# Performance work log

Measured on AMD Instinct MI355X. Metric: run time of the kernel, lower is better.

The kernel has to match this reference:

```python
import jax, jax.numpy as jnp
import numpy as np

N_NODES = 100000
N_EDGES = 2000000
N_GRAPHS = 2000
IN_DIM = 7
EDGE_DIM = 4
HID = 32
N_CLASSES = 2
NEG_SLOPE = 0.2
BN_EPS = 1e-5


def setup_inputs() -> dict:
    key = jax.random.key(0)
    ks = jax.random.split(key, 16)
    x = jax.random.normal(ks[0], (N_NODES, IN_DIM), dtype=jnp.float32)
    edge_index = jax.random.randint(ks[1], (2, N_EDGES), 0, N_NODES, dtype=jnp.int64)
    batch = jnp.sort(jax.random.randint(ks[2], (N_NODES,), 0, N_GRAPHS, dtype=jnp.int64))
    edge_attr = jax.random.normal(ks[3], (N_EDGES, EDGE_DIM), dtype=jnp.float32)
    s = 0.1
    W0 = jax.random.normal(ks[4], (IN_DIM, HID), dtype=jnp.float32) * s
    W12 = jax.random.normal(ks[5], (2, HID, HID), dtype=jnp.float32) * s
    att_src = jax.random.normal(ks[6], (3, HID), dtype=jnp.float32) * s
    att_dst = jax.random.normal(ks[7], (3, HID), dtype=jnp.float32) * s
    lin_edge = jax.random.normal(ks[8], (3, EDGE_DIM, HID), dtype=jnp.float32) * s
    att_edge = jax.random.normal(ks[9], (3, HID), dtype=jnp.float32) * s
    bias = jnp.zeros((3, HID), dtype=jnp.float32)
    bn_gamma = jnp.ones((3, HID), dtype=jnp.float32)
    bn_beta = jnp.zeros((3, HID), dtype=jnp.float32)
    fc_W = jax.random.normal(ks[10], (HID, N_CLASSES), dtype=jnp.float32) * s
    fc_b = jnp.zeros((N_CLASSES,), dtype=jnp.float32)
    return dict(x=x, edge_index=edge_index, batch=batch, edge_attr=edge_attr,
                W0=W0, W12=W12, att_src=att_src, att_dst=att_dst,
                lin_edge=lin_edge, att_edge=att_edge, bias=bias,
                bn_gamma=bn_gamma, bn_beta=bn_beta, fc_W=fc_W, fc_b=fc_b)


def gat_layer(x, src, dst, edge_attr, W, a_src, a_dst, We, a_edge, b):
    # PyG GATConv, heads=1, add_self_loops=False: edge_attr conditions attention only.
    N = x.shape[0]
    h = x @ W                                   # [N, H]
    e = edge_attr @ We                          # [E, H]
    score = ((h * a_src).sum(-1)[src]
             + (h * a_dst).sum(-1)[dst]
             + (e * a_edge).sum(-1))            # [E]
    score = jax.nn.leaky_relu(score, NEG_SLOPE)
    m = jax.ops.segment_max(score, dst, num_segments=N)
    w = jnp.exp(score - m[dst])
    denom = jax.ops.segment_sum(w, dst, num_segments=N)
    alpha = w / (denom[dst] + 1e-16)            # segment softmax over incoming edges
    out = jax.ops.segment_sum(h[src] * alpha[:, None], dst, num_segments=N)
    return out + b


def batchnorm(x, gamma, beta):
    mu = x.mean(axis=0)
    var = ((x - mu) ** 2).mean(axis=0)          # biased var, as torch BN normalization
    return (x - mu) * jax.lax.rsqrt(var + BN_EPS) * gamma + beta


def reference(x, edge_index, batch, edge_attr, W0, W12, att_src, att_dst,
              lin_edge, att_edge, bias, bn_gamma, bn_beta, fc_W, fc_b):
    src, dst = edge_index[0], edge_index[1]
    Ws = [W0, W12[0], W12[1]]
    h = x
    for l in range(3):
        h = gat_layer(h, src, dst, edge_attr, Ws[l], att_src[l], att_dst[l],
                      lin_edge[l], att_edge[l], bias[l])
        h = batchnorm(h, bn_gamma[l], bn_beta[l])
        h = jax.nn.relu(h)
    node_embs = h
    graph_emb = jax.ops.segment_sum(node_embs, batch, num_segments=N_GRAPHS)
    out = graph_emb @ fc_W + fc_b
    return (out, node_embs, graph_emb)
```

## Files before the change

### kernel.cpp

```cpp
#include <hip/hip_runtime.h>
#include <math.h>

#define N_NODES   100000
#define N_EDGES   2000000
#define N_GRAPHS  2000
#define IN_DIM    7
#define EDGE_DIM  4
#define HID       32
#define N_CLASSES 2
#define NEG_SLOPE 0.2f
#define BN_EPS    1e-5f

__global__ void k_ce_all(const float* __restrict__ lin_edge, const float* __restrict__ att_edge,
                         float* __restrict__ ce3, float* __restrict__ gsum3,
                         float* __restrict__ gsq3) {
    int t = threadIdx.x;
    if (t < 12) {
        int l = t >> 2, d = t & 3;
        float s = 0.f;
        for (int k = 0; k < HID; ++k)
            s += lin_edge[(size_t)l * EDGE_DIM * HID + d * HID + k] * att_edge[l * HID + k];
        ce3[t] = s;
    }
    if (t < 3 * HID) { gsum3[t] = 0.f; gsq3[t] = 0.f; }
}

__global__ void k_hist(const int* __restrict__ dst, int* __restrict__ deg) {
    int e = blockIdx.x * blockDim.x + threadIdx.x;
    if (e < N_EDGES) atomicAdd(deg + dst[e], 1);
}

__global__ void k_scan(const int* __restrict__ deg, int* __restrict__ offs,
                       int* __restrict__ cursor) {
    __shared__ int wsum[16];
    __shared__ int carry;
    int t = threadIdx.x, lane = t & 63, w = t >> 6;
    if (t == 0) carry = 0;
    __syncthreads();
    for (int base = 0; base < N_NODES; base += 1024) {
        int i = base + t;
        int v = (i < N_NODES) ? deg[i] : 0;
        int x = v;
#pragma unroll
        for (int o = 1; o < 64; o <<= 1) {
            int y = __shfl_up(x, o, 64);
            if (lane >= o) x += y;
        }
        if (lane == 63) wsum[w] = x;
        __syncthreads();
        if (t < 16) {
            int s = wsum[t];
#pragma unroll
            for (int o = 1; o < 16; o <<= 1) {
                int y = __shfl_up(s, o, 16);
                if (t >= o) s += y;
            }
            wsum[t] = s;
        }
        __syncthreads();
        int wpref = (w == 0) ? 0 : wsum[w - 1];
        int excl = carry + wpref + x - v;
        if (i < N_NODES) { offs[i] = excl; cursor[i] = excl; }
        __syncthreads();
        if (t == 0) carry += wsum[15];
        __syncthreads();
    }
}

__global__ void k_scatter(const int* __restrict__ src, const int* __restrict__ dst,
                          const float4* __restrict__ eattr, const float* __restrict__ ce3,
                          int* __restrict__ cursor, int4* __restrict__ pack) {
    int e = blockIdx.x * blockDim.x + threadIdx.x;
    if (e >= N_EDGES) return;
    float4 ea = eattr[e];
    float e0 = ea.x * ce3[0] + ea.y * ce3[1] + ea.z * ce3[2] + ea.w * ce3[3];
    float e1 = ea.x * ce3[4] + ea.y * ce3[5] + ea.z * ce3[6] + ea.w * ce3[7];
    float e2 = ea.x * ce3[8] + ea.y * ce3[9] + ea.z * ce3[10] + ea.w * ce3[11];
    int d = dst[e];
    int pos = atomicAdd(cursor + d, 1);
    pack[pos] = make_int4(src[e], __float_as_int(e0), __float_as_int(e1), __float_as_int(e2));
}

template <int INDIM, bool BN>
__global__ void k_linear(const float* __restrict__ in, const float* __restrict__ W,
                         const float* __restrict__ a_src, const float* __restrict__ a_dst,
                         const float* __restrict__ gsum, const float* __restrict__ gsq,
                         const float* __restrict__ gamma, const float* __restrict__ beta,
                         float* __restrict__ h, float* __restrict__ asrc,
                         float* __restrict__ adst) {
    __shared__ float Ws[INDIM * HID];
    for (int i = threadIdx.x; i < INDIM * HID; i += blockDim.x) Ws[i] = W[i];
    __syncthreads();
    int g = threadIdx.x >> 5, k = threadIdx.x & 31;
    int n = blockIdx.x * 8 + g;
    if (n >= N_NODES) return;
    float xv;
    if (BN) {
        const float invN = 1.f / (float)N_NODES;
        float mu = gsum[k] * invN;
        float var = gsq[k] * invN - mu * mu;
        var = fmaxf(var, 0.f);
        float scl = rsqrtf(var + BN_EPS) * gamma[k];
        float v = (in[(size_t)n * INDIM + k] - mu) * scl + beta[k];
        xv = fmaxf(v, 0.f);
    } else {
        xv = (k < INDIM) ? in[(size_t)n * INDIM + k] : 0.f;
    }
    float acc = 0.f;
#pragma unroll
    for (int d = 0; d < INDIM; ++d) acc += __shfl(xv, d, 32) * Ws[d * HID + k];
    h[(size_t)n * HID + k] = acc;
    float vs = acc * a_src[k];
    float vd = acc * a_dst[k];
#pragma unroll
    for (int m = 16; m > 0; m >>= 1) {
        vs += __shfl_xor(vs, m, 32);
        vd += __shfl_xor(vd, m, 32);
    }
    if (k == 0) { asrc[n] = vs; adst[n] = vd; }
}

template <int L>
__global__ void k_aggr(const int4* __restrict__ pack, const int* __restrict__ offs,
                       const int* __restrict__ endp, const float* __restrict__ h,
                       const float* __restrict__ asrc, const float* __restrict__ adst,
                       const float* __restrict__ bias, float* __restrict__ out,
                       float* __restrict__ gsum, float* __restrict__ gsq) {
    __shared__ float ssum[HID], ssq[HID];
    if (threadIdx.x < HID) { ssum[threadIdx.x] = 0.f; ssq[threadIdx.x] = 0.f; }
    __syncthreads();
    int g = threadIdx.x >> 5, k = threadIdx.x & 31;
    int n = blockIdx.x * 8 + g;
    if (n < N_NODES) {
        int p = offs[n], en = endp[n];
        float ad = adst[n];
        float m = -INFINITY, den = 0.f, a = 0.f;
        for (; p < en; ++p) {
            int4 pk = pack[p];
            int s = pk.x;
            float edot = __int_as_float(L == 0 ? pk.y : (L == 1 ? pk.z : pk.w));
            float sc = asrc[s] + ad + edot;
            sc = sc > 0.f ? sc : NEG_SLOPE * sc;
            float hv = h[(size_t)s * HID + k];
            if (sc <= m) {
                float wgt = __expf(sc - m);
                den += wgt;
                a = fmaf(wgt, hv, a);
            } else {
                float r = __expf(m - sc);
                den = fmaf(den, r, 1.f);
                a = fmaf(a, r, hv);
                m = sc;
            }
        }
        float v = a / (den + 1e-16f) + bias[k];
        out[(size_t)n * HID + k] = v;
        atomicAdd(&ssum[k], v);
        atomicAdd(&ssq[k], v * v);
    }
    __syncthreads();
    if (threadIdx.x < HID) {
        atomicAdd(gsum + threadIdx.x, ssum[threadIdx.x]);
        atomicAdd(gsq + threadIdx.x, ssq[threadIdx.x]);
    }
}

__global__ void k_bn_relu_pool(const float* __restrict__ acc, const float* __restrict__ gsum,
                               const float* __restrict__ gsq, const float* __restrict__ gamma,
                               const float* __restrict__ beta, const int* __restrict__ batch,
                               float* __restrict__ nemb, float* __restrict__ gemb) {
    int g = threadIdx.x >> 5, k = threadIdx.x & 31;
    int n = blockIdx.x * 8 + g;
    if (n >= N_NODES) return;
    const float invN = 1.f / (float)N_NODES;
    float mu = gsum[k] * invN;
    float var = gsq[k] * invN - mu * mu;
    var = fmaxf(var, 0.f);
    float scl = rsqrtf(var + BN_EPS) * gamma[k];
    float v = (acc[(size_t)n * HID + k] - mu) * scl + beta[k];
    v = fmaxf(v, 0.f);
    nemb[(size_t)n * HID + k] = v;
    atomicAdd(gemb + (size_t)batch[n] * HID + k, v);
}

__global__ void k_fc(const float* __restrict__ gemb, const float* __restrict__ W,
                     const float* __restrict__ b, float* __restrict__ out) {
    int g = blockIdx.x * blockDim.x + threadIdx.x;
    if (g >= N_GRAPHS) return;
    float a0 = b[0], a1 = b[1];
    for (int k = 0; k < HID; ++k) {
        float v = gemb[(size_t)g * HID + k];
        a0 += v * W[k * 2 + 0];
        a1 += v * W[k * 2 + 1];
    }
    out[g * 2 + 0] = a0;
    out[g * 2 + 1] = a1;
}

extern "C" void kernel_launch(void* const* d_in, const int* in_sizes, int n_in,
                              void* d_out, int out_size, void* d_ws, size_t ws_size,
                              hipStream_t stream) {
    const float* x        = (const float*)d_in[0];
    const int*   ei       = (const int*)d_in[1];
    const int*   batch    = (const int*)d_in[2];
    const float* eattr    = (const float*)d_in[3];
    const float* W0       = (const float*)d_in[4];
    const float* W12      = (const float*)d_in[5];
    const float* att_src  = (const float*)d_in[6];
    const float* att_dst  = (const float*)d_in[7];
    const float* lin_edge = (const float*)d_in[8];
    const float* att_edge = (const float*)d_in[9];
    const float* bias     = (const float*)d_in[10];
    const float* bn_gamma = (const float*)d_in[11];
    const float* bn_beta  = (const float*)d_in[12];
    const float* fc_W     = (const float*)d_in[13];
    const float* fc_b     = (const float*)d_in[14];

    const int* srcA = ei;
    const int* dstA = ei + N_EDGES;

    float* out       = (float*)d_out;
    float* node_embs = out + N_GRAPHS * N_CLASSES;
    float* graph_emb = node_embs + (size_t)N_NODES * HID;

    char* ws = (char*)d_ws;
    size_t off = 0;
    auto alloc = [&](size_t bytes) { char* p = ws + off; off += (bytes + 255) & ~(size_t)255; return p; };
    float* hT    = (float*)alloc((size_t)N_NODES * HID * 4);
    float* A0    = (float*)alloc((size_t)N_NODES * HID * 4);
    float* A1    = (float*)alloc((size_t)N_NODES * HID * 4);
    int4*  pack  = (int4*)alloc((size_t)N_EDGES * 16);
    int*   deg   = (int*)alloc((size_t)N_NODES * 4);
    int*   offs  = (int*)alloc((size_t)N_NODES * 4);
    int*   cursor= (int*)alloc((size_t)N_NODES * 4);
    float* asrc  = (float*)alloc((size_t)N_NODES * 4);
    float* adst  = (float*)alloc((size_t)N_NODES * 4);
    float* ce3   = (float*)alloc(12 * 4);
    float* gsum3 = (float*)alloc(3 * HID * 4);
    float* gsq3  = (float*)alloc(3 * HID * 4);
    (void)ws_size;

    const int nodeBlocks = (N_NODES + 7) / 8;
    const int edgeBlocks = (N_EDGES + 255) / 256;

    hipMemsetAsync(deg, 0, (size_t)N_NODES * 4, stream);
    k_ce_all<<<1, 128, 0, stream>>>(lin_edge, att_edge, ce3, gsum3, gsq3);
    k_hist<<<edgeBlocks, 256, 0, stream>>>(dstA, deg);
    k_scan<<<1, 1024, 0, stream>>>(deg, offs, cursor);
    k_scatter<<<edgeBlocks, 256, 0, stream>>>(srcA, dstA, (const float4*)eattr, ce3, cursor, pack);

    k_linear<IN_DIM, false><<<nodeBlocks, 256, 0, stream>>>(
        x, W0, att_src, att_dst, nullptr, nullptr, nullptr, nullptr, hT, asrc, adst);
    k_aggr<0><<<nodeBlocks, 256, 0, stream>>>(pack, offs, cursor, hT, asrc, adst,
                                              bias, A0, gsum3, gsq3);
    k_linear<HID, true><<<nodeBlocks, 256, 0, stream>>>(
        A0, W12, att_src + HID, att_dst + HID, gsum3, gsq3, bn_gamma, bn_beta, hT, asrc, adst);
    k_aggr<1><<<nodeBlocks, 256, 0, stream>>>(pack, offs, cursor, hT, asrc, adst,
                                              bias + HID, A1, gsum3 + HID, gsq3 + HID);
    k_linear<HID, true><<<nodeBlocks, 256, 0, stream>>>(
        A1, W12 + HID * HID, att_src + 2 * HID, att_dst + 2 * HID,
        gsum3 + HID, gsq3 + HID, bn_gamma + HID, bn_beta + HID, hT, asrc, adst);
    k_aggr<2><<<nodeBlocks, 256, 0, stream>>>(pack, offs, cursor, hT, asrc, adst,
                                              bias + 2 * HID, A0, gsum3 + 2 * HID, gsq3 + 2 * HID);

    hipMemsetAsync(graph_emb, 0, (size_t)N_GRAPHS * HID * 4, stream);
    k_bn_relu_pool<<<nodeBlocks, 256, 0, stream>>>(A0, gsum3 + 2 * HID, gsq3 + 2 * HID,
                                                   bn_gamma + 2 * HID, bn_beta + 2 * HID,
                                                   batch, node_embs, graph_emb);
    k_fc<<<(N_GRAPHS + 255) / 256, 256, 0, stream>>>(graph_emb, fc_W, fc_b, out);
}
```

Before: 1.115 ms.

## Batch edge gathers eight at a time and drop online softmax max

Restructures the per-node aggregation loop to load eight packed edges, their source scores and feature values up front before computing weights. This exposes more independent memory requests per thread so gather latency can overlap. The running-max online softmax is replaced by plain exp without max subtraction, which removes the branch and rescaling but risks overflow when attention scores are large. Tail edges are clamped to the last edge and masked to zero weight.

```diff
diff --git a/kernel.cpp b/kernel.cpp
--- a/kernel.cpp
+++ b/kernel.cpp
@@ -132,25 +132,33 @@
     int g = threadIdx.x >> 5, k = threadIdx.x & 31;
     int n = blockIdx.x * 8 + g;
     if (n < N_NODES) {
-        int p = offs[n], en = endp[n];
+        int pbeg = offs[n], en = endp[n];
         float ad = adst[n];
-        float m = -INFINITY, den = 0.f, a = 0.f;
-        for (; p < en; ++p) {
-            int4 pk = pack[p];
-            int s = pk.x;
-            float edot = __int_as_float(L == 0 ? pk.y : (L == 1 ? pk.z : pk.w));
-            float sc = asrc[s] + ad + edot;
-            sc = sc > 0.f ? sc : NEG_SLOPE * sc;
-            float hv = h[(size_t)s * HID + k];
-            if (sc <= m) {
-                float wgt = __expf(sc - m);
-                den += wgt;
-                a = fmaf(wgt, hv, a);
-            } else {
-                float r = __expf(m - sc);
-                den = fmaf(den, r, 1.f);
-                a = fmaf(a, r, hv);
-                m = sc;
+        float den = 0.f, a = 0.f;
+        for (int p = pbeg; p < en; p += 8) {
+            int4 pk[8];
+            float as[8], hh[8], w[8];
+#pragma unroll
+            for (int j = 0; j < 8; ++j) {
+                int q = p + j;
+                q = q < en ? q : en - 1;
+                pk[j] = pack[q];
+            }
+#pragma unroll
+            for (int j = 0; j < 8; ++j) as[j] = asrc[pk[j].x];
+#pragma unroll
+            for (int j = 0; j < 8; ++j) hh[j] = h[(size_t)pk[j].x * HID + k];
+#pragma unroll
+            for (int j = 0; j < 8; ++j) {
+                float edot = __int_as_float(L == 0 ? pk[j].y : (L == 1 ? pk[j].z : pk[j].w));
+                float sc = as[j] + ad + edot;
+                sc = sc > 0.f ? sc : NEG_SLOPE * sc;
+                w[j] = (p + j < en) ? __expf(sc) : 0.f;
+            }
+#pragma unroll
+            for (int j = 0; j < 8; ++j) {
+                den += w[j];
+                a = fmaf(w[j], hh[j], a);
             }
         }
         float v = a / (den + 1e-16f) + bias[k];
```

After: 1.020 ms. 1.09x faster.
